# Optimization experiments

Measured on AMD Instinct MI355X. Metric: run time of the kernel, lower is better.

## Reference

```python
import jax, jax.numpy as jnp
import numpy as np

IIR_LEN = 16384


def setup_inputs() -> dict:
    key = jax.random.key(0)
    k1, k2, k3, k4, k5 = jax.random.split(key, 5)
    N, C, L = 32, 2, 131072
    return {
        "input_signals": jax.random.normal(k1, (N, C, L), dtype=jnp.float32),
        "z_alpha": jax.random.normal(k2, (N, 1), dtype=jnp.float32),
        "log_threshold": jax.random.normal(k3, (N, 1), dtype=jnp.float32),
        "log_ratio": jax.random.normal(k4, (N, 1), dtype=jnp.float32),
        "log_knee": jax.random.normal(k5, (N, 1), dtype=jnp.float32),
    }


def reference(input_signals, z_alpha, log_threshold, log_ratio, log_knee):
    N, C, L = input_signals.shape
    # --- envelope follower: energy detection ---
    loudness = jnp.mean(jnp.square(input_signals), axis=-2)  # (N, L)
    # truncated one-pole IIR as causal FIR: h[n] = (1 - alpha) * alpha^n
    alpha = jax.nn.sigmoid(z_alpha)  # (N, 1)
    n = jnp.arange(IIR_LEN, dtype=jnp.float32)
    h = (1.0 - alpha) * jnp.power(alpha, n)  # (N, IIR_LEN)
    # causal linear convolution via FFT, keep first L samples
    fft_len = L + IIR_LEN
    env = jnp.fft.irfft(
        jnp.fft.rfft(loudness, n=fft_len) * jnp.fft.rfft(h, n=fft_len),
        n=fft_len,
    )[:, :L]
    log_energy = jnp.log(env + 1e-5)  # (N, L)
    # --- quadratic-knee gain (exp/softplus form) ---
    T = log_threshold - 6.0  # (N, 1)
    ratio = 1.0 + jnp.exp(log_ratio)  # (N, 1)
    knee = jnp.exp(log_knee - 1.0)  # (N, 1)
    log_gain = (1.0 / ratio - 1.0) * jax.nn.softplus(knee * (log_energy - T)) / knee
    gain = jnp.exp(log_gain)[:, None, :]  # (N, 1, L)
    return gain * input_signals
```

## Files before the change

### kernel.cpp

```cpp
#include <hip/hip_runtime.h>
#include <cmath>

#define LLEN 131072
#define IIRL 16384
#define CHUNK 16384
#define NBLK (LLEN / CHUNK)
#define TPB 1024
#define NW (TPB / 64)

typedef float floatx4 __attribute__((ext_vector_type(4)));

__device__ __forceinline__ float powiu(float b, unsigned e) {
    float r = 1.0f;
    while (e) { if (e & 1u) r *= b; b *= b; e >>= 1; }
    return r;
}

__device__ __forceinline__ float exp2_hw(float x) { return __builtin_amdgcn_exp2f(x); }
__device__ __forceinline__ float log2_hw(float x) { return __builtin_amdgcn_logf(x); }

__global__ __launch_bounds__(TPB) void k_fused(
    const float* __restrict__ x, const float* __restrict__ za,
    const float* __restrict__ lt, const float* __restrict__ lr,
    const float* __restrict__ lk, float* __restrict__ out)
{
    const int d     = blockIdx.y * gridDim.x + blockIdx.x;
    const int per   = (gridDim.x * gridDim.y) >> 3;
    const int w     = (d & 7) * per + (d >> 3);
    const int chunk = w % NBLK, n = w / NBLK;

    const int tid = threadIdx.x, lane = tid & 63, wid = tid >> 6;

    const float alpha = 1.0f / (1.0f + __expf(-za[n]));
    const float omah  = 0.5f * (1.0f - alpha);
    const float A16K  = powiu(alpha, IIRL);
    const float LOG2E = 1.4426950408889634f;
    const float Tthr  = lt[n] - 6.0f;
    const float ratio = 1.0f + __expf(lr[n]);
    const float knee  = __expf(lk[n] - 1.0f);
    const float coef  = (1.0f / ratio - 1.0f) / knee;
    const float C0    = -knee * Tthr * LOG2E;

    const float a4    = (alpha * alpha) * (alpha * alpha);
    const float a256  = powiu(a4, 64u);
    const float A1024 = powiu(a256, 4u);

    const long  base = (long)n * 2 * LLEN + (long)chunk * CHUNK;
    const float* x0 = x + base;
    const float* x1 = x0 + LLEN;
    const int woff = wid * 1024;

    float4 xa[4], xb[4];
    {
        const float4* p0 = reinterpret_cast<const float4*>(x0 + woff);
        const float4* p1 = reinterpret_cast<const float4*>(x1 + woff);
        #pragma unroll
        for (int q = 0; q < 4; ++q) {
            xa[q] = p0[q * 64 + lane];
            xb[q] = p1[q * 64 + lane];
        }
    }

    float b[4][4];
    #pragma unroll
    for (int q = 0; q < 4; ++q) {
        float4 a = xa[q], c = xb[q];
        b[q][0] = omah * fmaf(a.x, a.x, c.x * c.x);
        b[q][1] = omah * fmaf(a.y, a.y, c.y * c.y);
        b[q][2] = omah * fmaf(a.z, a.z, c.z * c.z);
        b[q][3] = omah * fmaf(a.w, a.w, c.w * c.w);
    }

    float rt[4];
    #pragma unroll
    for (int q = 0; q < 4; ++q) {
        float s = b[q][0];
        s = fmaf(alpha, s, b[q][1]);
        s = fmaf(alpha, s, b[q][2]);
        s = fmaf(alpha, s, b[q][3]);
        rt[q] = s;
    }

    float v0 = rt[0], v1 = rt[1], v2 = rt[2], v3 = rt[3];
    float g = a4;
    #pragma unroll
    for (int off = 1; off < 64; off <<= 1) {
        float y0 = __shfl_up(v0, off, 64);
        float y1 = __shfl_up(v1, off, 64);
        float y2 = __shfl_up(v2, off, 64);
        float y3 = __shfl_up(v3, off, 64);
        if (lane >= off) {
            v0 = fmaf(g, y0, v0); v1 = fmaf(g, y1, v1);
            v2 = fmaf(g, y2, v2); v3 = fmaf(g, y3, v3);
        }
        g *= g;
    }
    float Ex[4];
    Ex[0] = __shfl_up(v0, 1, 64); Ex[1] = __shfl_up(v1, 1, 64);
    Ex[2] = __shfl_up(v2, 1, 64); Ex[3] = __shfl_up(v3, 1, 64);
    if (lane == 0) { Ex[0] = Ex[1] = Ex[2] = Ex[3] = 0.0f; }
    float S[4];
    S[0] = __shfl(v0, 63, 64); S[1] = __shfl(v1, 63, 64);
    S[2] = __shfl(v2, 63, 64); S[3] = __shfl(v3, 63, 64);

    float W = S[0];
    W = fmaf(a256, W, S[1]); W = fmaf(a256, W, S[2]); W = fmaf(a256, W, S[3]);

    const float sc = A16K * omah;
    float uw = 0.0f;
    if (chunk > 0) {
        float4 pa[4], pb[4];
        const float4* r0 = reinterpret_cast<const float4*>(x0 - CHUNK + woff);
        const float4* r1 = reinterpret_cast<const float4*>(x1 - CHUNK + woff);
        #pragma unroll
        for (int q = 0; q < 4; ++q) {
            pa[q] = r0[q * 64 + lane];
            pb[q] = r1[q * 64 + lane];
        }
        float sq[4];
        #pragma unroll
        for (int q = 0; q < 4; ++q) {
            float4 ta = pa[q], tc = pb[q];
            float pl0 = fmaf(ta.x, ta.x, tc.x * tc.x);
            float pl1 = fmaf(ta.y, ta.y, tc.y * tc.y);
            float pl2 = fmaf(ta.z, ta.z, tc.z * tc.z);
            float pl3 = fmaf(ta.w, ta.w, tc.w * tc.w);
            float s = omah * pl0;
            s = fmaf(alpha, s, omah * pl1);
            s = fmaf(alpha, s, omah * pl2);
            s = fmaf(alpha, s, omah * pl3);
            sq[q] = s;
            if (A16K != 0.0f) {
                b[q][0] -= sc * pl0; b[q][1] -= sc * pl1;
                b[q][2] -= sc * pl2; b[q][3] -= sc * pl3;
            }
        }
        const float lw = powiu(a4, (unsigned)(63 - lane));
        float t0 = sq[0] * lw, t1 = sq[1] * lw, t2 = sq[2] * lw, t3 = sq[3] * lw;
        #pragma unroll
        for (int off = 32; off; off >>= 1) {
            t0 += __shfl_xor(t0, off, 64);
            t1 += __shfl_xor(t1, off, 64);
            t2 += __shfl_xor(t2, off, 64);
            t3 += __shfl_xor(t3, off, 64);
        }
        uw = t0;
        uw = fmaf(a256, uw, t1);
        uw = fmaf(a256, uw, t2);
        uw = fmaf(a256, uw, t3);
    }
    if (A16K != 0.0f && chunk > 0) {
        #pragma unroll
        for (int q = 0; q < 4; ++q) {
            float s = b[q][0];
            s = fmaf(alpha, s, b[q][1]);
            s = fmaf(alpha, s, b[q][2]);
            s = fmaf(alpha, s, b[q][3]);
            rt[q] = s;
        }
        v0 = rt[0]; v1 = rt[1]; v2 = rt[2]; v3 = rt[3];
        float g2 = a4;
        #pragma unroll
        for (int off = 1; off < 64; off <<= 1) {
            float y0 = __shfl_up(v0, off, 64);
            float y1 = __shfl_up(v1, off, 64);
            float y2 = __shfl_up(v2, off, 64);
            float y3 = __shfl_up(v3, off, 64);
            if (lane >= off) {
                v0 = fmaf(g2, y0, v0); v1 = fmaf(g2, y1, v1);
                v2 = fmaf(g2, y2, v2); v3 = fmaf(g2, y3, v3);
            }
            g2 *= g2;
        }
        Ex[0] = __shfl_up(v0, 1, 64); Ex[1] = __shfl_up(v1, 1, 64);
        Ex[2] = __shfl_up(v2, 1, 64); Ex[3] = __shfl_up(v3, 1, 64);
        if (lane == 0) { Ex[0] = Ex[1] = Ex[2] = Ex[3] = 0.0f; }
        S[0] = __shfl(v0, 63, 64); S[1] = __shfl(v1, 63, 64);
        S[2] = __shfl(v2, 63, 64); S[3] = __shfl(v3, 63, 64);
        W = S[0];
        W = fmaf(a256, W, S[1]); W = fmaf(a256, W, S[2]); W = fmaf(a256, W, S[3]);
    }

    __shared__ float wtB[NW], wtP[NW];
    if (lane == 0) { wtB[wid] = W; wtP[wid] = uw; }
    __syncthreads();

    float C = 0.0f;
    #pragma unroll
    for (int ww = 0; ww < NW; ++ww) C = fmaf(A1024, C, wtP[ww]);
    float wc = 0.0f;
    for (int ww = 0; ww < wid; ++ww) wc = fmaf(A1024, wc, wtB[ww]);

    const float e_wave = fmaf(powiu(A1024, (unsigned)wid), C, wc);
    const float a4l    = powiu(a4, (unsigned)lane);

    float cq = e_wave;
    floatx4* o0 = reinterpret_cast<floatx4*>(out + base + woff);
    floatx4* o1 = reinterpret_cast<floatx4*>(out + base + LLEN + woff);
    #pragma unroll
    for (int q = 0; q < 4; ++q) {
        float e = fmaf(a4l, cq, Ex[q]);
        cq = fmaf(a256, cq, S[q]);
        float4 a = xa[q], c = xb[q];
        floatx4 oa, ob;
        const float* ia = reinterpret_cast<const float*>(&a);
        const float* ib = reinterpret_cast<const float*>(&c);
        #pragma unroll
        for (int m = 0; m < 4; ++m) {
            e = fmaf(alpha, e, b[q][m]);
            float t  = fmaf(knee, log2_hw(e + 1e-5f), C0);
            float u  = exp2_hw(t);
            float sp = log2_hw(1.0f + u);
            float gain = exp2_hw(coef * sp);
            oa[m] = gain * ia[m];
            ob[m] = gain * ib[m];
        }
        __builtin_nontemporal_store(oa, &o0[q * 64 + lane]);
        __builtin_nontemporal_store(ob, &o1[q * 64 + lane]);
    }
}

extern "C" void kernel_launch(void* const* d_in, const int* in_sizes, int n_in,
                              void* d_out, int out_size, void* d_ws, size_t ws_size,
                              hipStream_t stream) {
    const float* x  = (const float*)d_in[0];
    const float* za = (const float*)d_in[1];
    const float* lt = (const float*)d_in[2];
    const float* lr = (const float*)d_in[3];
    const float* lk = (const float*)d_in[4];
    float* out = (float*)d_out;

    const int N = in_sizes[1];
    dim3 grid(NBLK, N), block(TPB);
    k_fused<<<grid, block, 0, stream>>>(x, za, lt, lr, lk, out);
}
```

Measured before the change: 15.53 us.

## Pass inter-chunk carry through global flags instead of re-reading previous chunk

When alpha^16384 underflows to zero, each block publishes its local block sum to a workspace slot using a release store with a ready flag. The next chunk spin-waits on that slot to get its carry. This avoids reloading and re-reducing the previous 16K-sample chunk, which was a large share of the input traffic. In exchange it adds a memset launch, a dependency between blocks that assumes they are co-resident, and spin-wait latency; the general path is kept when alpha^16384 is nonzero.

Result: slower. 23.13 us (+48.9%).

```diff
diff --git a/kernel.cpp b/kernel.cpp
--- a/kernel.cpp
+++ b/kernel.cpp
@@ -1,5 +1,6 @@
 #include <hip/hip_runtime.h>
 #include <cmath>
+#include <cstdint>
 
 #define LLEN 131072
 #define IIRL 16384
@@ -22,7 +23,8 @@
 __global__ __launch_bounds__(TPB) void k_fused(
     const float* __restrict__ x, const float* __restrict__ za,
     const float* __restrict__ lt, const float* __restrict__ lr,
-    const float* __restrict__ lk, float* __restrict__ out)
+    const float* __restrict__ lk, uint64_t* __restrict__ P,
+    float* __restrict__ out)
 {
     const int d     = blockIdx.y * gridDim.x + blockIdx.x;
     const int per   = (gridDim.x * gridDim.y) >> 3;
@@ -50,6 +52,9 @@
     const float* x1 = x0 + LLEN;
     const int woff = wid * 1024;
 
+    __shared__ float wtB[NW], wtP[NW];
+    __shared__ float carry_s;
+
     float4 xa[4], xb[4];
     {
         const float4* p0 = reinterpret_cast<const float4*>(x0 + woff);
@@ -106,50 +111,71 @@
     float W = S[0];
     W = fmaf(a256, W, S[1]); W = fmaf(a256, W, S[2]); W = fmaf(a256, W, S[3]);
 
-    const float sc = A16K * omah;
-    float uw = 0.0f;
-    if (chunk > 0) {
-        float4 pa[4], pb[4];
-        const float4* r0 = reinterpret_cast<const float4*>(x0 - CHUNK + woff);
-        const float4* r1 = reinterpret_cast<const float4*>(x1 - CHUNK + woff);
-        #pragma unroll
-        for (int q = 0; q < 4; ++q) {
-            pa[q] = r0[q * 64 + lane];
-            pb[q] = r1[q * 64 + lane];
-        }
-        float sq[4];
-        #pragma unroll
-        for (int q = 0; q < 4; ++q) {
-            float4 ta = pa[q], tc = pb[q];
-            float pl0 = fmaf(ta.x, ta.x, tc.x * tc.x);
-            float pl1 = fmaf(ta.y, ta.y, tc.y * tc.y);
-            float pl2 = fmaf(ta.z, ta.z, tc.z * tc.z);
-            float pl3 = fmaf(ta.w, ta.w, tc.w * tc.w);
-            float s = omah * pl0;
-            s = fmaf(alpha, s, omah * pl1);
-            s = fmaf(alpha, s, omah * pl2);
-            s = fmaf(alpha, s, omah * pl3);
-            sq[q] = s;
-            if (A16K != 0.0f) {
+    if (lane == 0) wtB[wid] = W;
+    __syncthreads();
+
+    float C;
+    if (A16K == 0.0f) {
+        if (tid == 0) {
+            if (chunk + 1 < NBLK) {
+                float Wblk = 0.0f;
+                #pragma unroll
+                for (int ww = 0; ww < NW; ++ww) Wblk = fmaf(A1024, Wblk, wtB[ww]);
+                const uint64_t pk = (1ull << 32) | (uint64_t)__float_as_uint(Wblk);
+                __hip_atomic_store(&P[n * NBLK + chunk], pk,
+                                   __ATOMIC_RELEASE, __HIP_MEMORY_SCOPE_AGENT);
+            }
+            if (chunk == 0) {
+                carry_s = 0.0f;
+            } else {
+                uint64_t e;
+                for (;;) {
+                    e = __hip_atomic_load(&P[n * NBLK + chunk - 1],
+                                          __ATOMIC_ACQUIRE, __HIP_MEMORY_SCOPE_AGENT);
+                    if (e >> 32) break;
+                    __builtin_amdgcn_s_sleep(2);
+                }
+                carry_s = __uint_as_float((uint32_t)(e & 0xffffffffu));
+            }
+        }
+        __syncthreads();
+        C = carry_s;
+    } else {
+        const float sc = A16K * omah;
+        float uw = 0.0f;
+        if (chunk > 0) {
+            const float4* r0 = reinterpret_cast<const float4*>(x0 - CHUNK + woff);
+            const float4* r1 = reinterpret_cast<const float4*>(x1 - CHUNK + woff);
+            float sq[4];
+            #pragma unroll
+            for (int q = 0; q < 4; ++q) {
+                float4 ta = r0[q * 64 + lane], tc = r1[q * 64 + lane];
+                float pl0 = fmaf(ta.x, ta.x, tc.x * tc.x);
+                float pl1 = fmaf(ta.y, ta.y, tc.y * tc.y);
+                float pl2 = fmaf(ta.z, ta.z, tc.z * tc.z);
+                float pl3 = fmaf(ta.w, ta.w, tc.w * tc.w);
+                float s = omah * pl0;
+                s = fmaf(alpha, s, omah * pl1);
+                s = fmaf(alpha, s, omah * pl2);
+                s = fmaf(alpha, s, omah * pl3);
+                sq[q] = s;
                 b[q][0] -= sc * pl0; b[q][1] -= sc * pl1;
                 b[q][2] -= sc * pl2; b[q][3] -= sc * pl3;
             }
-        }
-        const float lw = powiu(a4, (unsigned)(63 - lane));
-        float t0 = sq[0] * lw, t1 = sq[1] * lw, t2 = sq[2] * lw, t3 = sq[3] * lw;
-        #pragma unroll
-        for (int off = 32; off; off >>= 1) {
-            t0 += __shfl_xor(t0, off, 64);
-            t1 += __shfl_xor(t1, off, 64);
-            t2 += __shfl_xor(t2, off, 64);
-            t3 += __shfl_xor(t3, off, 64);
-        }
-        uw = t0;
-        uw = fmaf(a256, uw, t1);
-        uw = fmaf(a256, uw, t2);
-        uw = fmaf(a256, uw, t3);
-    }
-    if (A16K != 0.0f && chunk > 0) {
+            const float lw = powiu(a4, (unsigned)(63 - lane));
+            float t0 = sq[0] * lw, t1 = sq[1] * lw, t2 = sq[2] * lw, t3 = sq[3] * lw;
+            #pragma unroll
+            for (int off = 32; off; off >>= 1) {
+                t0 += __shfl_xor(t0, off, 64);
+                t1 += __shfl_xor(t1, off, 64);
+                t2 += __shfl_xor(t2, off, 64);
+                t3 += __shfl_xor(t3, off, 64);
+            }
+            uw = t0;
+            uw = fmaf(a256, uw, t1);
+            uw = fmaf(a256, uw, t2);
+            uw = fmaf(a256, uw, t3);
+        }
         #pragma unroll
         for (int q = 0; q < 4; ++q) {
             float s = b[q][0];
@@ -179,15 +205,13 @@
         S[2] = __shfl(v2, 63, 64); S[3] = __shfl(v3, 63, 64);
         W = S[0];
         W = fmaf(a256, W, S[1]); W = fmaf(a256, W, S[2]); W = fmaf(a256, W, S[3]);
-    }
-
-    __shared__ float wtB[NW], wtP[NW];
-    if (lane == 0) { wtB[wid] = W; wtP[wid] = uw; }
-    __syncthreads();
-
-    float C = 0.0f;
-    #pragma unroll
-    for (int ww = 0; ww < NW; ++ww) C = fmaf(A1024, C, wtP[ww]);
+        if (lane == 0) { wtB[wid] = W; wtP[wid] = uw; }
+        __syncthreads();
+        C = 0.0f;
+        #pragma unroll
+        for (int ww = 0; ww < NW; ++ww) C = fmaf(A1024, C, wtP[ww]);
+    }
+
     float wc = 0.0f;
     for (int ww = 0; ww < wid; ++ww) wc = fmaf(A1024, wc, wtB[ww]);
 
@@ -229,8 +253,10 @@
     const float* lr = (const float*)d_in[3];
     const float* lk = (const float*)d_in[4];
     float* out = (float*)d_out;
+    uint64_t* P = (uint64_t*)d_ws;
 
     const int N = in_sizes[1];
+    hipMemsetAsync(P, 0, (size_t)N * NBLK * sizeof(uint64_t), stream);
     dim3 grid(NBLK, N), block(TPB);
-    k_fused<<<grid, block, 0, stream>>>(x, za, lt, lr, lk, out);
+    k_fused<<<grid, block, 0, stream>>>(x, za, lt, lr, lk, P, out);
 }
```
